# Kernel optimization log

Hardware: AMD Instinct MI355X
Metric: run time of the kernel (lower is better)

## Reference

```python
import jax, jax.numpy as jnp
import numpy as np

B, T, N = 8, 1024, 1024
R, NR = 8, 128          # regions, neurons per region (N = R*NR)
D = 512                 # d_model


def setup_inputs() -> dict:
    key = jax.random.key(0)
    ks = jax.random.split(key, 6)
    spikes = jax.random.normal(ks[0], (B, T, N), dtype=jnp.float32)
    # region assignment: random permutation of neuron ids split into R groups
    perm = jax.random.permutation(ks[1], N)
    region_indices = perm.reshape(R, NR).astype(jnp.int32)
    # per-region Linear(NR -> D) stored already transposed for gathered layout
    W_enc = jax.random.normal(ks[2], (R, NR, D), dtype=jnp.float32) / np.sqrt(NR)
    b_enc = jax.random.normal(ks[3], (R, D), dtype=jnp.float32) * 0.02
    # per-region Linear(D -> NR)
    W_dec = jax.random.normal(ks[4], (R, D, NR), dtype=jnp.float32) / np.sqrt(D)
    b_dec = jax.random.normal(ks[5], (R, NR), dtype=jnp.float32) * 0.02
    return {"spikes": spikes, "W_enc": W_enc, "b_enc": b_enc,
            "W_dec": W_dec, "b_dec": b_dec, "region_indices": region_indices}


def reference(spikes, W_enc, b_enc, W_dec, b_dec, region_indices):
    # gather: per-region channel subsets  [B,T,R,NR]
    x_r = spikes[:, :, region_indices]
    # RegionEncoder: Linear(NR -> D) per region  [B,T,R,D]
    tokens = jnp.einsum('btrn,rnd->btrd', x_r, W_enc) + b_enc
    # RegionDecoder: Linear(D -> NR) per region  [B,T,R,NR]
    y = jnp.einsum('btrd,rdn->btrn', tokens, W_dec) + b_dec
    # scatter back into full neuron axis (index_copy_ on dim 2)
    flat_idx = region_indices.reshape(-1)          # [N], a permutation
    out = jnp.zeros_like(spikes).at[:, :, flat_idx].set(y.reshape(spikes.shape[0], spikes.shape[1], -1))
    return out
```

## Files before the change

kernel.cpp:

```cpp
#include <hip/hip_runtime.h>


typedef __attribute__((ext_vector_type(8))) short bf16x8;
typedef __attribute__((ext_vector_type(4))) float f32x4;
typedef __attribute__((ext_vector_type(4))) short s16x4;

#define NREG 8
#define NRD  128
#define DD   512
#define NN   1024
#define ROWS 16

static __device__ __forceinline__ unsigned short f2bf(float x) {
  union { float f; unsigned u; } v; v.f = x;
  unsigned r = v.u + 0x7fffu + ((v.u >> 16) & 1u);
  return (unsigned short)(r >> 16);
}
static __device__ __forceinline__ float bf2f(unsigned short b) {
  union { unsigned u; float f; } v; v.u = ((unsigned)b) << 16;
  return v.f;
}

__global__ __launch_bounds__(256) void prep1_kernel(
    const float* __restrict__ W_enc, const float* __restrict__ b_enc,
    const float* __restrict__ W_dec, const int* __restrict__ idx,
    int* __restrict__ pos_ws, float* __restrict__ part,
    float* __restrict__ part_c)
{
  __shared__ unsigned short As[128 * 128];
  __shared__ unsigned short Bs[128 * 128];
  int blk = blockIdx.x, t = threadIdx.x;

  if (blk < 32) {
    int r = blk >> 2, dc = blk & 3, d0 = dc * 128;
    const float* We = W_enc + (size_t)r * NRD * DD;
    const float* Wd = W_dec + (size_t)r * DD * NRD;
    const float* be = b_enc + (size_t)r * DD;

    int n4 = (t & 31) * 4, dlb = t >> 5;
    float c0 = 0.f, c1 = 0.f, c2 = 0.f, c3 = 0.f;
    #pragma unroll
    for (int p = 0; p < 16; ++p) {
      int dl = dlb + p * 8;
      float4 v = *(const float4*)&Wd[(size_t)(d0 + dl) * NRD + n4];
      float bev = be[d0 + dl];
      As[(n4 + 0) * 128 + (dl ^ (((n4 + 0) & 7) << 3))] = f2bf(v.x);
      As[(n4 + 1) * 128 + (dl ^ (((n4 + 1) & 7) << 3))] = f2bf(v.y);
      As[(n4 + 2) * 128 + (dl ^ (((n4 + 2) & 7) << 3))] = f2bf(v.z);
      As[(n4 + 3) * 128 + (dl ^ (((n4 + 3) & 7) << 3))] = f2bf(v.w);
      c0 += v.x * bev; c1 += v.y * bev; c2 += v.z * bev; c3 += v.w * bev;
    }
    {
      float4 cv; cv.x = c0; cv.y = c1; cv.z = c2; cv.w = c3;
      *(float4*)&part_c[((size_t)(r * 4 + dc) * 8 + dlb) * 128 + n4] = cv;
    }
    #pragma unroll
    for (int i = 0; i < 8; ++i) {
      int cid = t + i * 256;
      int k = cid >> 4, dq = (cid & 15) * 8;
      const float* src = &We[(size_t)k * DD + d0 + dq];
      float4 u = *(const float4*)src;
      float4 u2 = *(const float4*)(src + 4);
      bf16x8 pk;
      pk[0] = (short)f2bf(u.x);  pk[1] = (short)f2bf(u.y);
      pk[2] = (short)f2bf(u.z);  pk[3] = (short)f2bf(u.w);
      pk[4] = (short)f2bf(u2.x); pk[5] = (short)f2bf(u2.y);
      pk[6] = (short)f2bf(u2.z); pk[7] = (short)f2bf(u2.w);
      *(bf16x8*)&Bs[k * 128 + (dq ^ ((k & 7) << 3))] = pk;
    }
    __syncthreads();

    int lane = t & 63, w = t >> 6;
    int arow = lane & 15, ag = lane >> 4;
    f32x4 acc[8][2];
    #pragma unroll
    for (int i = 0; i < 8; ++i) {
      acc[i][0] = (f32x4){0.f, 0.f, 0.f, 0.f};
      acc[i][1] = (f32x4){0.f, 0.f, 0.f, 0.f};
    }
    #pragma unroll
    for (int nt = 0; nt < 8; ++nt) {
      int nl = nt * 16 + arow, asw = (nl & 7) << 3;
      bf16x8 a[4];
      #pragma unroll
      for (int ks = 0; ks < 4; ++ks)
        a[ks] = *(const bf16x8*)&As[nl * 128 + ((ks * 32 + ag * 8) ^ asw)];
      #pragma unroll
      for (int kt = 0; kt < 2; ++kt) {
        int kk = w * 32 + kt * 16 + arow, bsw = (kk & 7) << 3;
        #pragma unroll
        for (int ks = 0; ks < 4; ++ks) {
          bf16x8 b = *(const bf16x8*)&Bs[kk * 128 + ((ks * 32 + ag * 8) ^ bsw)];
          acc[nt][kt] = __builtin_amdgcn_mfma_f32_16x16x32_bf16(a[ks], b, acc[nt][kt], 0, 0, 0);
        }
      }
    }
    float* dst = part + (size_t)(r * 4 + dc) * 16384;
    #pragma unroll
    for (int nt = 0; nt < 8; ++nt)
      #pragma unroll
      for (int kt = 0; kt < 2; ++kt)
        #pragma unroll
        for (int v = 0; v < 4; ++v)
          dst[(nt * 16 + ag * 4 + v) * 128 + (w * 32 + kt * 16 + arow)] = acc[nt][kt][v];
  } else {
    #pragma unroll
    for (int i = 0; i < 4; ++i) {
      int q = t * 4 + i;
      pos_ws[idx[q]] = q;
    }
  }
}

__global__ __launch_bounds__(256) void prep2_kernel(
    const float* __restrict__ part, const float* __restrict__ part_c,
    const float* __restrict__ b_dec, unsigned short* __restrict__ MT_ws,
    float* __restrict__ c_ws)
{
  int blk = blockIdx.x, t = threadIdx.x;
  if (blk < 128) {
    int e0 = (blk * 256 + t) * 4;
    int r = e0 >> 14, off = e0 & 16383;
    const float* p = part + (size_t)r * 4 * 16384 + off;
    float4 s0 = *(const float4*)&p[0];
    float4 s1 = *(const float4*)&p[16384];
    float4 s2 = *(const float4*)&p[32768];
    float4 s3 = *(const float4*)&p[49152];
    s16x4 o;
    o.x = (short)f2bf(s0.x + s1.x + s2.x + s3.x);
    o.y = (short)f2bf(s0.y + s1.y + s2.y + s3.y);
    o.z = (short)f2bf(s0.z + s1.z + s2.z + s3.z);
    o.w = (short)f2bf(s0.w + s1.w + s2.w + s3.w);
    *(s16x4*)&MT_ws[e0] = o;
  } else if (blk < 132) {
    int e = (blk - 128) * 256 + t;
    int n = e & 127;
    int r = e >> 7;
    float s = b_dec[e];
    #pragma unroll
    for (int dc = 0; dc < 4; ++dc)
      #pragma unroll
      for (int g = 0; g < 8; ++g)
        s += part_c[((size_t)(r * 4 + dc) * 8 + g) * 128 + n];
    c_ws[e] = s;
  }
}

__global__ __launch_bounds__(512) void codec_kernel(
    const float* __restrict__ spikes, const int* __restrict__ pos_ws,
    const float* __restrict__ c_ws, const unsigned short* __restrict__ MT_ws,
    float* __restrict__ out)
{
  __shared__ unsigned short Xs[ROWS * NN];
  __shared__ unsigned short Ys[ROWS * NN];
  int t = threadIdx.x;
  int w = t >> 6, lane = t & 63;
  int arow = lane & 15, ag = lane >> 4;
  int n0 = w * 16 + arow;
  size_t row0 = (size_t)blockIdx.x * ROWS;

  int4 p4c[4];
  #pragma unroll
  for (int ch = 0; ch < 4; ++ch)
    p4c[ch] = *(const int4*)&pos_ws[ch * 256 + lane * 4];
  float cv[NREG];
  #pragma unroll
  for (int r = 0; r < NREG; ++r)
    cv[r] = c_ws[r * 128 + n0];

  #pragma unroll
  for (int ch = 0; ch < 4; ++ch) {
    int j = ch * 256 + lane * 4;
    int4 p4 = p4c[ch];
    #pragma unroll
    for (int rl = 0; rl < 2; ++rl) {
      int row = w * 2 + rl;
      float4 v = *(const float4*)&spikes[(row0 + row) * NN + j];
      int base = row * NN, sw = (row & 7) << 3;
      Xs[base + (p4.x ^ sw)] = f2bf(v.x);
      Xs[base + (p4.y ^ sw)] = f2bf(v.y);
      Xs[base + (p4.z ^ sw)] = f2bf(v.z);
      Xs[base + (p4.w ^ sw)] = f2bf(v.w);
    }
  }
  __syncthreads();

  int asw = (arow & 7) << 3;
  #pragma unroll
  for (int r = 0; r < NREG; ++r) {
    bf16x8 a[4];
    #pragma unroll
    for (int kt = 0; kt < 4; ++kt)
      a[kt] = *(const bf16x8*)&Xs[arow * NN + ((r * 128 + kt * 32 + ag * 8) ^ asw)];
    const bf16x8* b = (const bf16x8*)(MT_ws + (size_t)(r * 128 + n0) * 128 + ag * 8);
    f32x4 acc = {0.f, 0.f, 0.f, 0.f};
    #pragma unroll
    for (int kt = 0; kt < 4; ++kt)
      acc = __builtin_amdgcn_mfma_f32_16x16x32_bf16(a[kt], b[kt * 4], acc, 0, 0, 0);
    #pragma unroll
    for (int v = 0; v < 4; ++v) {
      int i = ag * 4 + v, isw = (i & 7) << 3;
      Ys[i * NN + ((r * 128 + n0) ^ isw)] = f2bf(acc[v] + cv[r]);
    }
  }
  __syncthreads();

  #pragma unroll
  for (int ch = 0; ch < 4; ++ch) {
    int j = ch * 256 + lane * 4;
    int4 p4 = p4c[ch];
    #pragma unroll
    for (int rl = 0; rl < 2; ++rl) {
      int row = w * 2 + rl;
      int base = row * NN, sw = (row & 7) << 3;
      float4 v;
      v.x = bf2f(Ys[base + (p4.x ^ sw)]);
      v.y = bf2f(Ys[base + (p4.y ^ sw)]);
      v.z = bf2f(Ys[base + (p4.z ^ sw)]);
      v.w = bf2f(Ys[base + (p4.w ^ sw)]);
      *(float4*)&out[(row0 + row) * NN + j] = v;
    }
  }
}

extern "C" void kernel_launch(void* const* d_in, const int* in_sizes, int n_in,
                              void* d_out, int out_size, void* d_ws, size_t ws_size,
                              hipStream_t stream) {
  const float* spikes = (const float*)d_in[0];
  const float* W_enc  = (const float*)d_in[1];
  const float* b_enc  = (const float*)d_in[2];
  const float* W_dec  = (const float*)d_in[3];
  const float* b_dec  = (const float*)d_in[4];
  const int*   idx    = (const int*)d_in[5];
  float* out = (float*)d_out;

  char* ws = (char*)d_ws;
  int*            pos_ws  = (int*)ws;
  float*          c_ws    = (float*)(ws + 4096);
  unsigned short* MT_ws   = (unsigned short*)(ws + 8192);
  float*          part    = (float*)(ws + 270336);
  float*          part_c  = (float*)(ws + 2367488);

  prep1_kernel<<<33, 256, 0, stream>>>(W_enc, b_enc, W_dec, idx,
                                       pos_ws, part, part_c);
  prep2_kernel<<<132, 256, 0, stream>>>(part, part_c, b_dec, MT_ws, c_ws);
  codec_kernel<<<8192 / ROWS, 512, 0, stream>>>(spikes, pos_ws, c_ws, MT_ws, out);
}
```

Measured before the change: 39.65 us.

## Process two row tiles per block with software-pipelined spike loads

Each codec block now handles two 16-row subtiles. It prefetches the second tile's spikes into registers while the first tile's MFMA runs, and overlaps the first tile's output stores with the second tile's compute. This halves the grid (256 blocks) and raises LDS use per block to about 96KB, which limits occupancy. The manual bf16 rounding is also swapped for the HIP intrinsic conversion.

Measured after the change: 39.72 us. No clear change (+0.2%).

```diff
diff --git a/kernel.cpp b/kernel.cpp
--- a/kernel.cpp
+++ b/kernel.cpp
@@ -1,4 +1,5 @@
 #include <hip/hip_runtime.h>
+#include <hip/hip_bf16.h>
 
 
 typedef __attribute__((ext_vector_type(8))) short bf16x8;
@@ -10,11 +11,17 @@
 #define DD   512
 #define NN   1024
 #define ROWS 16
+#define SUBT 2
 
 static __device__ __forceinline__ unsigned short f2bf(float x) {
   union { float f; unsigned u; } v; v.f = x;
   unsigned r = v.u + 0x7fffu + ((v.u >> 16) & 1u);
   return (unsigned short)(r >> 16);
+}
+static __device__ __forceinline__ unsigned short f2bf_hw(float x) {
+  union { __hip_bfloat16 h; unsigned short u; } c;
+  c.h = __float2bfloat16(x);
+  return c.u;
 }
 static __device__ __forceinline__ float bf2f(unsigned short b) {
   union { unsigned u; float f; } v; v.u = ((unsigned)b) << 16;
@@ -151,13 +158,14 @@
     const float* __restrict__ c_ws, const unsigned short* __restrict__ MT_ws,
     float* __restrict__ out)
 {
-  __shared__ unsigned short Xs[ROWS * NN];
+  __shared__ unsigned short Xs[SUBT][ROWS * NN];
   __shared__ unsigned short Ys[ROWS * NN];
   int t = threadIdx.x;
   int w = t >> 6, lane = t & 63;
   int arow = lane & 15, ag = lane >> 4;
   int n0 = w * 16 + arow;
-  size_t row0 = (size_t)blockIdx.x * ROWS;
+  int asw = (arow & 7) << 3;
+  size_t row0 = (size_t)blockIdx.x * (ROWS * SUBT);
 
   int4 p4c[4];
   #pragma unroll
@@ -177,21 +185,27 @@
       int row = w * 2 + rl;
       float4 v = *(const float4*)&spikes[(row0 + row) * NN + j];
       int base = row * NN, sw = (row & 7) << 3;
-      Xs[base + (p4.x ^ sw)] = f2bf(v.x);
-      Xs[base + (p4.y ^ sw)] = f2bf(v.y);
-      Xs[base + (p4.z ^ sw)] = f2bf(v.z);
-      Xs[base + (p4.w ^ sw)] = f2bf(v.w);
+      Xs[0][base + (p4.x ^ sw)] = f2bf_hw(v.x);
+      Xs[0][base + (p4.y ^ sw)] = f2bf_hw(v.y);
+      Xs[0][base + (p4.z ^ sw)] = f2bf_hw(v.z);
+      Xs[0][base + (p4.w ^ sw)] = f2bf_hw(v.w);
     }
   }
   __syncthreads();
 
-  int asw = (arow & 7) << 3;
+  float4 pv[4][2];
+  #pragma unroll
+  for (int ch = 0; ch < 4; ++ch)
+    #pragma unroll
+    for (int rl = 0; rl < 2; ++rl)
+      pv[ch][rl] = *(const float4*)&spikes[(row0 + ROWS + w * 2 + rl) * NN + ch * 256 + lane * 4];
+
   #pragma unroll
   for (int r = 0; r < NREG; ++r) {
     bf16x8 a[4];
     #pragma unroll
     for (int kt = 0; kt < 4; ++kt)
-      a[kt] = *(const bf16x8*)&Xs[arow * NN + ((r * 128 + kt * 32 + ag * 8) ^ asw)];
+      a[kt] = *(const bf16x8*)&Xs[0][arow * NN + ((r * 128 + kt * 32 + ag * 8) ^ asw)];
     const bf16x8* b = (const bf16x8*)(MT_ws + (size_t)(r * 128 + n0) * 128 + ag * 8);
     f32x4 acc = {0.f, 0.f, 0.f, 0.f};
     #pragma unroll
@@ -200,11 +214,39 @@
     #pragma unroll
     for (int v = 0; v < 4; ++v) {
       int i = ag * 4 + v, isw = (i & 7) << 3;
-      Ys[i * NN + ((r * 128 + n0) ^ isw)] = f2bf(acc[v] + cv[r]);
+      Ys[i * NN + ((r * 128 + n0) ^ isw)] = f2bf_hw(acc[v] + cv[r]);
+    }
+  }
+
+  #pragma unroll
+  for (int ch = 0; ch < 4; ++ch) {
+    int4 p4 = p4c[ch];
+    #pragma unroll
+    for (int rl = 0; rl < 2; ++rl) {
+      int row = w * 2 + rl;
+      int base = row * NN, sw = (row & 7) << 3;
+      float4 v = pv[ch][rl];
+      Xs[1][base + (p4.x ^ sw)] = f2bf_hw(v.x);
+      Xs[1][base + (p4.y ^ sw)] = f2bf_hw(v.y);
+      Xs[1][base + (p4.z ^ sw)] = f2bf_hw(v.z);
+      Xs[1][base + (p4.w ^ sw)] = f2bf_hw(v.w);
     }
   }
   __syncthreads();
 
+  f32x4 accr[NREG];
+  #pragma unroll
+  for (int r = 0; r < NREG; ++r) {
+    bf16x8 a[4];
+    #pragma unroll
+    for (int kt = 0; kt < 4; ++kt)
+      a[kt] = *(const bf16x8*)&Xs[1][arow * NN + ((r * 128 + kt * 32 + ag * 8) ^ asw)];
+    const bf16x8* b = (const bf16x8*)(MT_ws + (size_t)(r * 128 + n0) * 128 + ag * 8);
+    accr[r] = (f32x4){0.f, 0.f, 0.f, 0.f};
+    #pragma unroll
+    for (int kt = 0; kt < 4; ++kt)
+      accr[r] = __builtin_amdgcn_mfma_f32_16x16x32_bf16(a[kt], b[kt * 4], accr[r], 0, 0, 0);
+  }
   #pragma unroll
   for (int ch = 0; ch < 4; ++ch) {
     int j = ch * 256 + lane * 4;
@@ -219,6 +261,33 @@
       v.z = bf2f(Ys[base + (p4.z ^ sw)]);
       v.w = bf2f(Ys[base + (p4.w ^ sw)]);
       *(float4*)&out[(row0 + row) * NN + j] = v;
+    }
+  }
+  __syncthreads();
+
+  #pragma unroll
+  for (int r = 0; r < NREG; ++r)
+    #pragma unroll
+    for (int v = 0; v < 4; ++v) {
+      int i = ag * 4 + v, isw = (i & 7) << 3;
+      Ys[i * NN + ((r * 128 + n0) ^ isw)] = f2bf_hw(accr[r][v] + cv[r]);
+    }
+  __syncthreads();
+
+  #pragma unroll
+  for (int ch = 0; ch < 4; ++ch) {
+    int j = ch * 256 + lane * 4;
+    int4 p4 = p4c[ch];
+    #pragma unroll
+    for (int rl = 0; rl < 2; ++rl) {
+      int row = w * 2 + rl;
+      int base = row * NN, sw = (row & 7) << 3;
+      float4 v;
+      v.x = bf2f(Ys[base + (p4.x ^ sw)]);
+      v.y = bf2f(Ys[base + (p4.y ^ sw)]);
+      v.z = bf2f(Ys[base + (p4.z ^ sw)]);
+      v.w = bf2f(Ys[base + (p4.w ^ sw)]);
+      *(float4*)&out[(row0 + ROWS + row) * NN + j] = v;
     }
   }
 }
@@ -244,5 +313,5 @@
   prep1_kernel<<<33, 256, 0, stream>>>(W_enc, b_enc, W_dec, idx,
                                        pos_ws, part, part_c);
   prep2_kernel<<<132, 256, 0, stream>>>(part, part_c, b_dec, MT_ws, c_ws);
-  codec_kernel<<<8192 / ROWS, 512, 0, stream>>>(spikes, pos_ws, c_ws, MT_ws, out);
-}
+  codec_kernel<<<8192 / (ROWS * SUBT), 512, 0, stream>>>(spikes, pos_ws, c_ws, MT_ws, out);
+}
```
